# Kernel tuning notes

Hardware: AMD Instinct MI355X
Metric: run time of the kernel (lower is better)

## Reference

```python
import jax, jax.numpy as jnp
import numpy as np

TAU = 1.0  # current_temp buffer (temperature=1.0)

def setup_inputs() -> dict:
    key = jax.random.key(0)
    ks = jax.random.split(key, 6)
    B, T, d, L, H = 4, 64, 128, 32, 32  # H = hidden_dim // 2
    z_signal = jax.random.normal(ks[0], (B, T, d, L), dtype=jnp.float32)
    W_mag = jax.random.normal(ks[1], (d, d), dtype=jnp.float32) * 0.01  # init_scale
    W1 = jax.random.normal(ks[2], (H, 2 * L), dtype=jnp.float32) * (1.0 / np.sqrt(2 * L))
    b1 = jax.random.normal(ks[3], (H,), dtype=jnp.float32) * 0.01
    W2 = jax.random.normal(ks[4], (1, H), dtype=jnp.float32) * (1.0 / np.sqrt(H))
    b2 = jax.random.normal(ks[5], (1,), dtype=jnp.float32) * 0.01
    return {"z_signal": z_signal, "W_mag": W_mag, "W1": W1, "b1": b1, "W2": W2, "b2": b2}

def reference(z_signal, W_mag, W1, b1, W2, b2):
    B, T, d, L = z_signal.shape
    h = z_signal.reshape(B * T, d, L)  # [N, d, L]
    # Linear(2L,H) on cat(h_i, h_j) == h_i @ W1a.T + h_j @ W1b.T (decomposed, same math)
    W1a, W1b = W1[:, :L], W1[:, L:]
    pa = jnp.einsum('ndl,hl->ndh', h, W1a)  # contribution of h_i
    pb = jnp.einsum('ndl,hl->ndh', h, W1b)  # contribution of h_j
    hidden = jax.nn.relu(pa[:, :, None, :] + pb[:, None, :, :] + b1)  # [N, d, d, H]
    scores = jnp.einsum('nijh,h->nij', hidden, W2[0]) + b2[0]          # [N, d, d]
    antisym = scores - jnp.swapaxes(scores, -1, -2)
    antisym_logits = antisym.mean(axis=0)                              # [d, d]
    eye = jnp.eye(d, dtype=z_signal.dtype)
    dir_probs = jax.nn.sigmoid(antisym_logits / TAU) * (1.0 - eye)
    # symmetric magnitude with zero diagonal
    Wm = 0.5 * (W_mag + W_mag.T) * (1.0 - eye)
    A = jax.nn.sigmoid(Wm) * dir_probs * (1.0 - eye)
    return (A, Wm)
```

## Files before the change

### kernel.cpp

```cpp
#include <hip/hip_runtime.h>
#include <hip/hip_bf16.h>
#include <math.h>

#define D    128
#define NT   256
#define HD   32
#define LD   32
#define PADW 132

static __device__ inline unsigned short f2bf(float f) {
    __hip_bfloat16 b = __float2bfloat16(f);
    return *reinterpret_cast<unsigned short*>(&b);
}
static __device__ inline float bf2f(unsigned int u16v) {
    union { unsigned int i; float f; } v;
    v.i = u16v << 16;
    return v.f;
}

union SmemA {
    float zt[LD][PADW];
    float lin[2][D];
};
union SmemB {
    struct { float spa[HD][PADW]; float spb[HD][PADW]; } p;
    unsigned short st[D][PADW];
};

__global__ __launch_bounds__(512) void fused_pab_scores(
    const float* __restrict__ z, const float* __restrict__ W1,
    const float* __restrict__ b1, const float* __restrict__ W2,
    unsigned short* __restrict__ Dp)
{
    __shared__ SmemA sa;
    __shared__ SmemB sb;

    const int t = threadIdx.x;
    const int n = blockIdx.x;

    {
        const float4* zsrc = (const float4*)(z + (size_t)n * (D * LD));
        #pragma unroll
        for (int q = 0; q < 2; ++q) {
            int f = t + q * 512;
            float4 v = zsrc[f];
            int i = f >> 3;
            int l = (f & 7) * 4;
            sa.zt[l + 0][i] = v.x; sa.zt[l + 1][i] = v.y;
            sa.zt[l + 2][i] = v.z; sa.zt[l + 3][i] = v.w;
        }
    }

    const int h  = t & 31;
    const int iq = t >> 5;
    float wa[LD], wb[LD];
    #pragma unroll
    for (int k = 0; k < 8; ++k) {
        *(float4*)&wa[k*4] = *(const float4*)&W1[h * 64 + k*4];
        *(float4*)&wb[k*4] = *(const float4*)&W1[h * 64 + 32 + k*4];
    }
    const float bias = b1[h];
    __syncthreads();

    {
        float a[8], c[8];
        #pragma unroll
        for (int r = 0; r < 8; ++r) { a[r] = bias; c[r] = 0.f; }
        #pragma unroll
        for (int l = 0; l < LD; ++l) {
            float4 z0 = *(const float4*)&sa.zt[l][iq * 8];
            float4 z1 = *(const float4*)&sa.zt[l][iq * 8 + 4];
            float zr[8] = {z0.x, z0.y, z0.z, z0.w, z1.x, z1.y, z1.z, z1.w};
            #pragma unroll
            for (int r = 0; r < 8; ++r) {
                a[r] = fmaf(zr[r], wa[l], a[r]);
                c[r] = fmaf(zr[r], wb[l], c[r]);
            }
        }
        *(float4*)&sb.p.spa[h][iq * 8]     = make_float4(a[0], a[1], a[2], a[3]);
        *(float4*)&sb.p.spa[h][iq * 8 + 4] = make_float4(a[4], a[5], a[6], a[7]);
        *(float4*)&sb.p.spb[h][iq * 8]     = make_float4(c[0], c[1], c[2], c[3]);
        *(float4*)&sb.p.spb[h][iq * 8 + 4] = make_float4(c[4], c[5], c[6], c[7]);
    }

    float w2r[HD];
    #pragma unroll
    for (int q = 0; q < HD; ++q) w2r[q] = 0.5f * W2[q];
    __syncthreads();

    if (t < 256) {
        const int kind = t >> 7, i2 = t & 127;
        float s = 0.f;
        #pragma unroll
        for (int hq = 0; hq < HD; ++hq) {
            float v = kind ? sb.p.spb[hq][i2] : sb.p.spa[hq][i2];
            s = fmaf(w2r[hq], v, s);
        }
        sa.lin[kind][i2] = s;
    }

    const int tx = t & 31;
    const int ty = t >> 5;
    float acc[8][4];
    #pragma unroll
    for (int r = 0; r < 8; ++r)
        #pragma unroll
        for (int c = 0; c < 4; ++c) acc[r][c] = 0.f;

    #pragma unroll 4
    for (int hh = 0; hh < HD; ++hh) {
        float4 a0 = *(const float4*)&sb.p.spa[hh][ty * 8];
        float4 a1 = *(const float4*)&sb.p.spa[hh][ty * 8 + 4];
        float4 bv = *(const float4*)&sb.p.spb[hh][tx * 4];
        const float w = w2r[hh];
        float ar[8] = {a0.x, a0.y, a0.z, a0.w, a1.x, a1.y, a1.z, a1.w};
        float br[4] = {bv.x, bv.y, bv.z, bv.w};
        #pragma unroll
        for (int r = 0; r < 8; ++r)
            #pragma unroll
            for (int c = 0; c < 4; ++c)
                acc[r][c] = fmaf(w, fabsf(ar[r] + br[c]), acc[r][c]);
    }
    __syncthreads();

    {
        float cai[8], cbj[4];
        #pragma unroll
        for (int r = 0; r < 8; ++r) cai[r] = sa.lin[0][ty * 8 + r];
        #pragma unroll
        for (int c = 0; c < 4; ++c) cbj[c] = sa.lin[1][tx * 4 + c];
        #pragma unroll
        for (int r = 0; r < 8; ++r)
            #pragma unroll
            for (int c = 0; c < 4; ++c)
                acc[r][c] += cai[r] + cbj[c];
    }

    #pragma unroll
    for (int r = 0; r < 8; ++r) {
        unsigned int p0 = ((unsigned int)f2bf(acc[r][1]) << 16) | f2bf(acc[r][0]);
        unsigned int p1 = ((unsigned int)f2bf(acc[r][3]) << 16) | f2bf(acc[r][2]);
        *(uint2*)&sb.st[ty * 8 + r][tx * 4] = make_uint2(p0, p1);
    }
    __syncthreads();

    unsigned short* Dn = Dp + (size_t)n * (D * D);
    #pragma unroll
    for (int half = 0; half < 2; ++half) {
        const int iq4 = ty * 2 + half;
        float dre[4][4];
        #pragma unroll
        for (int c = 0; c < 4; ++c) {
            int j = tx * 4 + c;
            uint2 tv = *(const uint2*)&sb.st[j][iq4 * 4];
            dre[0][c] = acc[half * 4 + 0][c] - bf2f(tv.x & 0xffff);
            dre[1][c] = acc[half * 4 + 1][c] - bf2f(tv.x >> 16);
            dre[2][c] = acc[half * 4 + 2][c] - bf2f(tv.y & 0xffff);
            dre[3][c] = acc[half * 4 + 3][c] - bf2f(tv.y >> 16);
        }
        #pragma unroll
        for (int r = 0; r < 4; ++r) {
            unsigned int p0 = ((unsigned int)f2bf(dre[r][1]) << 16) | f2bf(dre[r][0]);
            unsigned int p1 = ((unsigned int)f2bf(dre[r][3]) << 16) | f2bf(dre[r][2]);
            *(uint2*)&Dn[(iq4 * 4 + r) * D + tx * 4] = make_uint2(p0, p1);
        }
    }
}

__global__ __launch_bounds__(256) void finalize_kernel(
    const unsigned short* __restrict__ Dp, const float* __restrict__ Wmag,
    float* __restrict__ out)
{
    __shared__ float red[16][68];

    const int t    = threadIdx.x;
    const int row  = blockIdx.x >> 1;
    const int half = blockIdx.x & 1;
    const int g    = t >> 4;
    const int jq   = t & 15;
    const int jloc = jq * 4;

    float a4[4] = {0.f, 0.f, 0.f, 0.f};
    #pragma unroll 4
    for (int q = 0; q < 16; ++q) {
        int nn = g * 16 + q;
        uint2 u = *(const uint2*)&Dp[(size_t)nn * (D * D) + row * D + half * 64 + jloc];
        a4[0] += bf2f(u.x & 0xffff); a4[1] += bf2f(u.x >> 16);
        a4[2] += bf2f(u.y & 0xffff); a4[3] += bf2f(u.y >> 16);
    }
    *(float4*)&red[g][jloc] = make_float4(a4[0], a4[1], a4[2], a4[3]);
    __syncthreads();

    if (t < 64) {
        const int j = half * 64 + t;
        float s = 0.f;
        #pragma unroll
        for (int gg = 0; gg < 16; ++gg) s += red[gg][t];

        const int idx = row * D + j;
        float av  = s * (1.0f / 256.0f);
        float dir = 1.0f / (1.0f + __expf(-av));
        float wm  = 0.5f * (Wmag[row * D + j] + Wmag[j * D + row]);
        float A;
        if (row == j) { wm = 0.f; A = 0.f; }
        else          { A = dir / (1.0f + __expf(-wm)); }
        out[idx]         = A;
        out[D * D + idx] = wm;
    }
}

extern "C" void kernel_launch(void* const* d_in, const int* in_sizes, int n_in,
                              void* d_out, int out_size, void* d_ws, size_t ws_size,
                              hipStream_t stream)
{
    const float* z    = (const float*)d_in[0];
    const float* Wmag = (const float*)d_in[1];
    const float* W1   = (const float*)d_in[2];
    const float* b1   = (const float*)d_in[3];
    const float* W2   = (const float*)d_in[4];

    unsigned short* Dp = (unsigned short*)d_ws;
    float* out = (float*)d_out;

    fused_pab_scores<<<NT, 512, 0, stream>>>(z, W1, b1, W2, Dp);
    finalize_kernel<<<NT, 256, 0, stream>>>(Dp, Wmag, out);
}
```

Before: 30.12 us.

## Exploit antisymmetry: store only upper-triangle tiles and derive lower half in finalize

The score kernel now writes only the upper-triangular 8x8 tiles of the antisymmetric difference matrix into a packed slab, roughly halving the intermediate bf16 traffic. The finalize kernel reduces one tile per block and writes both (i,j) and (j,i) outputs, using sigmoid(-x)=1-sigmoid(x) and the symmetry of Wm. The first kernel moves to 256 threads with larger 8x8 register tiles per thread and an XOR-swizzled transpose buffer, trading more registers and less parallelism for fewer LDS loads per FMA. Half the threads sit idle during the write-out phase.

Result: no change. 30.13 us (+0.0%).

```diff
diff --git a/kernel.cpp b/kernel.cpp
--- a/kernel.cpp
+++ b/kernel.cpp
@@ -2,11 +2,14 @@
 #include <hip/hip_bf16.h>
 #include <math.h>
 
-#define D    128
-#define NT   256
-#define HD   32
-#define LD   32
-#define PADW 132
+#define D     128
+#define NT    256
+#define HD    32
+#define LD    32
+#define PADW  132
+#define STW   136
+#define TILES 136
+#define NSLAB (TILES * 64)
 
 static __device__ inline unsigned short f2bf(float f) {
     __hip_bfloat16 b = __float2bfloat16(f);
@@ -24,10 +27,10 @@
 };
 union SmemB {
     struct { float spa[HD][PADW]; float spb[HD][PADW]; } p;
-    unsigned short st[D][PADW];
+    unsigned short st[D][STW];
 };
 
-__global__ __launch_bounds__(512) void fused_pab_scores(
+__global__ __launch_bounds__(256) void fused_pab_scores(
     const float* __restrict__ z, const float* __restrict__ W1,
     const float* __restrict__ b1, const float* __restrict__ W2,
     unsigned short* __restrict__ Dp)
@@ -41,8 +44,8 @@
     {
         const float4* zsrc = (const float4*)(z + (size_t)n * (D * LD));
         #pragma unroll
-        for (int q = 0; q < 2; ++q) {
-            int f = t + q * 512;
+        for (int q = 0; q < 4; ++q) {
+            int f = t + q * 256;
             float4 v = zsrc[f];
             int i = f >> 3;
             int l = (f & 7) * 4;
@@ -51,8 +54,8 @@
         }
     }
 
-    const int h  = t & 31;
-    const int iq = t >> 5;
+    const int h   = t & 31;
+    const int isl = t >> 5;
     float wa[LD], wb[LD];
     #pragma unroll
     for (int k = 0; k < 8; ++k) {
@@ -63,24 +66,26 @@
     __syncthreads();
 
     {
-        float a[8], c[8];
-        #pragma unroll
-        for (int r = 0; r < 8; ++r) { a[r] = bias; c[r] = 0.f; }
+        float a[16], c[16];
+        #pragma unroll
+        for (int r = 0; r < 16; ++r) { a[r] = bias; c[r] = 0.f; }
         #pragma unroll
         for (int l = 0; l < LD; ++l) {
-            float4 z0 = *(const float4*)&sa.zt[l][iq * 8];
-            float4 z1 = *(const float4*)&sa.zt[l][iq * 8 + 4];
-            float zr[8] = {z0.x, z0.y, z0.z, z0.w, z1.x, z1.y, z1.z, z1.w};
-            #pragma unroll
-            for (int r = 0; r < 8; ++r) {
+            float zr[16];
+            #pragma unroll
+            for (int k = 0; k < 4; ++k)
+                *(float4*)&zr[k*4] = *(const float4*)&sa.zt[l][isl * 16 + k*4];
+            #pragma unroll
+            for (int r = 0; r < 16; ++r) {
                 a[r] = fmaf(zr[r], wa[l], a[r]);
                 c[r] = fmaf(zr[r], wb[l], c[r]);
             }
         }
-        *(float4*)&sb.p.spa[h][iq * 8]     = make_float4(a[0], a[1], a[2], a[3]);
-        *(float4*)&sb.p.spa[h][iq * 8 + 4] = make_float4(a[4], a[5], a[6], a[7]);
-        *(float4*)&sb.p.spb[h][iq * 8]     = make_float4(c[0], c[1], c[2], c[3]);
-        *(float4*)&sb.p.spb[h][iq * 8 + 4] = make_float4(c[4], c[5], c[6], c[7]);
+        #pragma unroll
+        for (int k = 0; k < 4; ++k) {
+            *(float4*)&sb.p.spa[h][isl * 16 + k*4] = *(float4*)&a[k*4];
+            *(float4*)&sb.p.spb[h][isl * 16 + k*4] = *(float4*)&c[k*4];
+        }
     }
 
     float w2r[HD];
@@ -88,7 +93,7 @@
     for (int q = 0; q < HD; ++q) w2r[q] = 0.5f * W2[q];
     __syncthreads();
 
-    if (t < 256) {
+    {
         const int kind = t >> 7, i2 = t & 127;
         float s = 0.f;
         #pragma unroll
@@ -99,113 +104,137 @@
         sa.lin[kind][i2] = s;
     }
 
-    const int tx = t & 31;
-    const int ty = t >> 5;
-    float acc[8][4];
+    const int tx = t & 15;
+    const int ty = t >> 4;
+    float acc[8][8];
     #pragma unroll
     for (int r = 0; r < 8; ++r)
         #pragma unroll
-        for (int c = 0; c < 4; ++c) acc[r][c] = 0.f;
-
-    #pragma unroll 4
+        for (int c = 0; c < 8; ++c) acc[r][c] = 0.f;
+
+    #pragma unroll 2
     for (int hh = 0; hh < HD; ++hh) {
-        float4 a0 = *(const float4*)&sb.p.spa[hh][ty * 8];
-        float4 a1 = *(const float4*)&sb.p.spa[hh][ty * 8 + 4];
-        float4 bv = *(const float4*)&sb.p.spb[hh][tx * 4];
+        float ar[8], br[8];
+        *(float4*)&ar[0] = *(const float4*)&sb.p.spa[hh][ty * 8];
+        *(float4*)&ar[4] = *(const float4*)&sb.p.spa[hh][ty * 8 + 4];
+        *(float4*)&br[0] = *(const float4*)&sb.p.spb[hh][tx * 8];
+        *(float4*)&br[4] = *(const float4*)&sb.p.spb[hh][tx * 8 + 4];
         const float w = w2r[hh];
-        float ar[8] = {a0.x, a0.y, a0.z, a0.w, a1.x, a1.y, a1.z, a1.w};
-        float br[4] = {bv.x, bv.y, bv.z, bv.w};
         #pragma unroll
         for (int r = 0; r < 8; ++r)
             #pragma unroll
-            for (int c = 0; c < 4; ++c)
+            for (int c = 0; c < 8; ++c)
                 acc[r][c] = fmaf(w, fabsf(ar[r] + br[c]), acc[r][c]);
     }
     __syncthreads();
 
     {
-        float cai[8], cbj[4];
+        float cai[8], cbj[8];
         #pragma unroll
         for (int r = 0; r < 8; ++r) cai[r] = sa.lin[0][ty * 8 + r];
         #pragma unroll
-        for (int c = 0; c < 4; ++c) cbj[c] = sa.lin[1][tx * 4 + c];
+        for (int c = 0; c < 8; ++c) cbj[c] = sa.lin[1][tx * 8 + c];
         #pragma unroll
         for (int r = 0; r < 8; ++r)
             #pragma unroll
-            for (int c = 0; c < 4; ++c)
+            for (int c = 0; c < 8; ++c)
                 acc[r][c] += cai[r] + cbj[c];
     }
 
-    #pragma unroll
-    for (int r = 0; r < 8; ++r) {
-        unsigned int p0 = ((unsigned int)f2bf(acc[r][1]) << 16) | f2bf(acc[r][0]);
-        unsigned int p1 = ((unsigned int)f2bf(acc[r][3]) << 16) | f2bf(acc[r][2]);
-        *(uint2*)&sb.st[ty * 8 + r][tx * 4] = make_uint2(p0, p1);
-    }
-    __syncthreads();
-
-    unsigned short* Dn = Dp + (size_t)n * (D * D);
-    #pragma unroll
-    for (int half = 0; half < 2; ++half) {
-        const int iq4 = ty * 2 + half;
-        float dre[4][4];
-        #pragma unroll
-        for (int c = 0; c < 4; ++c) {
-            int j = tx * 4 + c;
-            uint2 tv = *(const uint2*)&sb.st[j][iq4 * 4];
-            dre[0][c] = acc[half * 4 + 0][c] - bf2f(tv.x & 0xffff);
-            dre[1][c] = acc[half * 4 + 1][c] - bf2f(tv.x >> 16);
-            dre[2][c] = acc[half * 4 + 2][c] - bf2f(tv.y & 0xffff);
-            dre[3][c] = acc[half * 4 + 3][c] - bf2f(tv.y >> 16);
-        }
-        #pragma unroll
-        for (int r = 0; r < 4; ++r) {
-            unsigned int p0 = ((unsigned int)f2bf(dre[r][1]) << 16) | f2bf(dre[r][0]);
-            unsigned int p1 = ((unsigned int)f2bf(dre[r][3]) << 16) | f2bf(dre[r][2]);
-            *(uint2*)&Dn[(iq4 * 4 + r) * D + tx * 4] = make_uint2(p0, p1);
-        }
-    }
-}
-
-__global__ __launch_bounds__(256) void finalize_kernel(
+    {
+        const int physW = (tx ^ (ty & 7)) * 8;
+        #pragma unroll
+        for (int r = 0; r < 8; ++r) {
+            unsigned int pk[4];
+            #pragma unroll
+            for (int k = 0; k < 4; ++k)
+                pk[k] = ((unsigned int)f2bf(acc[r][2*k+1]) << 16) | f2bf(acc[r][2*k]);
+            *(uint4*)&sb.st[ty * 8 + r][physW] = *(uint4*)pk;
+        }
+    }
+    __syncthreads();
+
+    if (tx >= ty) {
+        float sji[8][8];
+        const int physR = (ty ^ (tx & 7)) * 8;
+        #pragma unroll
+        for (int c = 0; c < 8; ++c) {
+            uint4 u = *(const uint4*)&sb.st[tx * 8 + c][physR];
+            unsigned int xs[4] = {u.x, u.y, u.z, u.w};
+            #pragma unroll
+            for (int k = 0; k < 4; ++k) {
+                sji[c][2*k]   = bf2f(xs[k] & 0xffff);
+                sji[c][2*k+1] = bf2f(xs[k] >> 16);
+            }
+        }
+        const int tidx = ty * 16 - (ty * (ty - 1)) / 2 + (tx - ty);
+        unsigned short* Dn = Dp + (size_t)n * NSLAB + tidx * 64;
+        #pragma unroll
+        for (int r = 0; r < 8; ++r) {
+            unsigned int pk[4];
+            #pragma unroll
+            for (int k = 0; k < 4; ++k) {
+                unsigned short lo = f2bf(acc[r][2*k]   - sji[2*k][r]);
+                unsigned short hi = f2bf(acc[r][2*k+1] - sji[2*k+1][r]);
+                pk[k] = ((unsigned int)hi << 16) | lo;
+            }
+            *(uint4*)&Dn[r * 8] = *(uint4*)pk;
+        }
+    }
+}
+
+__global__ __launch_bounds__(256) void finalize_tiles(
     const unsigned short* __restrict__ Dp, const float* __restrict__ Wmag,
     float* __restrict__ out)
 {
-    __shared__ float red[16][68];
-
-    const int t    = threadIdx.x;
-    const int row  = blockIdx.x >> 1;
-    const int half = blockIdx.x & 1;
-    const int g    = t >> 4;
-    const int jq   = t & 15;
-    const int jloc = jq * 4;
-
-    float a4[4] = {0.f, 0.f, 0.f, 0.f};
-    #pragma unroll 4
-    for (int q = 0; q < 16; ++q) {
-        int nn = g * 16 + q;
-        uint2 u = *(const uint2*)&Dp[(size_t)nn * (D * D) + row * D + half * 64 + jloc];
-        a4[0] += bf2f(u.x & 0xffff); a4[1] += bf2f(u.x >> 16);
-        a4[2] += bf2f(u.y & 0xffff); a4[3] += bf2f(u.y >> 16);
-    }
-    *(float4*)&red[g][jloc] = make_float4(a4[0], a4[1], a4[2], a4[3]);
+    __shared__ float red[32][72];
+
+    const int b = blockIdx.x;
+    int tq = 0, base = 0;
+    while (b >= base + (16 - tq)) { base += 16 - tq; ++tq; }
+    const int tp = tq + (b - base);
+
+    const int t = threadIdx.x;
+    const int g = t >> 3;
+    const int s = t & 7;
+
+    float a8[8] = {0.f, 0.f, 0.f, 0.f, 0.f, 0.f, 0.f, 0.f};
+    #pragma unroll 2
+    for (int q = 0; q < 8; ++q) {
+        const int nn = g * 8 + q;
+        uint4 u = *(const uint4*)&Dp[(size_t)nn * NSLAB + b * 64 + s * 8];
+        unsigned int xs[4] = {u.x, u.y, u.z, u.w};
+        #pragma unroll
+        for (int k = 0; k < 4; ++k) {
+            a8[2*k]   += bf2f(xs[k] & 0xffff);
+            a8[2*k+1] += bf2f(xs[k] >> 16);
+        }
+    }
+    *(float4*)&red[g][s * 8]     = make_float4(a8[0], a8[1], a8[2], a8[3]);
+    *(float4*)&red[g][s * 8 + 4] = make_float4(a8[4], a8[5], a8[6], a8[7]);
     __syncthreads();
 
     if (t < 64) {
-        const int j = half * 64 + t;
-        float s = 0.f;
-        #pragma unroll
-        for (int gg = 0; gg < 16; ++gg) s += red[gg][t];
-
-        const int idx = row * D + j;
-        float av  = s * (1.0f / 256.0f);
-        float dir = 1.0f / (1.0f + __expf(-av));
-        float wm  = 0.5f * (Wmag[row * D + j] + Wmag[j * D + row]);
-        float A;
-        if (row == j) { wm = 0.f; A = 0.f; }
-        else          { A = dir / (1.0f + __expf(-wm)); }
-        out[idx]         = A;
-        out[D * D + idx] = wm;
+        const int r = t >> 3, c = t & 7;
+        float sum = 0.f;
+        #pragma unroll 8
+        for (int gg = 0; gg < 32; ++gg) sum += red[gg][t];
+
+        const int i = 8 * tq + r;
+        const int j = 8 * tp + c;
+        if (i == j) {
+            out[i * D + i]         = 0.f;
+            out[D * D + i * D + i] = 0.f;
+        } else if (j > i) {
+            float av  = sum * (1.0f / 256.0f);
+            float dir = 1.0f / (1.0f + __expf(-av));
+            float wmm = 0.5f * (Wmag[i * D + j] + Wmag[j * D + i]);
+            float sw  = 1.0f / (1.0f + __expf(-wmm));
+            out[i * D + j]         = dir * sw;
+            out[j * D + i]         = (1.0f - dir) * sw;
+            out[D * D + i * D + j] = wmm;
+            out[D * D + j * D + i] = wmm;
+        }
     }
 }
 
@@ -222,6 +251,6 @@
     unsigned short* Dp = (unsigned short*)d_ws;
     float* out = (float*)d_out;
 
-    fused_pab_scores<<<NT, 512, 0, stream>>>(z, W1, b1, W2, Dp);
-    finalize_kernel<<<NT, 256, 0, stream>>>(Dp, Wmag, out);
-}
+    fused_pab_scores<<<NT, 256, 0, stream>>>(z, W1, b1, W2, Dp);
+    finalize_tiles<<<TILES, 256, 0, stream>>>(Dp, Wmag, out);
+}
```
